# Performance work log

Measured on AMD Instinct MI355X. Metric: run time of the kernel, lower is better.

The kernel has to match this reference:

```python
import jax, jax.numpy as jnp
import numpy as np

# Model dims (match init_kwargs)
B, S, H = 1, 2048, 1024
E = 16            # n_routed_experts
I = 768           # moe_intermediate_size
TOPK = 4          # num_experts_per_tok
G = 4             # n_group
TOPK_G = 2        # topk_group
SCALE = 2.5       # routed_scaling_factor
N_SHARED = 1      # n_shared_experts


def setup_inputs() -> dict:
    key = jax.random.key(0)
    ks = jax.random.split(key, 9)
    def rn(k, shape, scale=0.02):
        return jax.random.normal(k, shape, dtype=jnp.float32) * scale
    return dict(
        hidden_states=jax.random.normal(ks[0], (B, S, H), dtype=jnp.float32),
        gate_w=rn(ks[1], (E, H)),
        gate_bias=jax.random.normal(ks[2], (E,), dtype=jnp.float32) * 0.1,
        w1=rn(ks[3], (E, I, H)),   # gate_proj weights [out,in]
        w2=rn(ks[4], (E, H, I)),   # down_proj weights
        w3=rn(ks[5], (E, I, H)),   # up_proj weights
        ws1=rn(ks[6], (I * N_SHARED, H)),
        ws2=rn(ks[7], (H, I * N_SHARED)),
        ws3=rn(ks[8], (I * N_SHARED, H)),
    )


def _route(x, gate_w, gate_bias):
    """noaux_tc routing: sigmoid scores + bias, group top-k, top_k experts."""
    n = x.shape[0]
    logits = jnp.einsum('nh,eh->ne', x.astype(jnp.float32), gate_w)  # [N,E]
    scores = jax.nn.sigmoid(logits)
    sb = scores + gate_bias                                          # biased scores
    # group score = sum of top-2 biased scores in each group
    gs = sb.reshape(n, G, E // G)
    group_scores = jnp.sum(jax.lax.top_k(gs, 2)[0], axis=-1)         # [N,G]
    _, gidx = jax.lax.top_k(group_scores, TOPK_G)                    # [N,TOPK_G]
    gmask = jnp.sum(jax.nn.one_hot(gidx, G, dtype=sb.dtype), axis=1) # [N,G]
    emask = jnp.repeat(gmask, E // G, axis=-1)                       # [N,E]
    masked = jnp.where(emask > 0, sb, -jnp.inf)
    _, tidx = jax.lax.top_k(masked, TOPK)                            # [N,TOPK]
    w = jnp.take_along_axis(scores, tidx, axis=1)                    # unbiased weights
    w = w / (jnp.sum(w, axis=-1, keepdims=True) + 1e-20)             # norm_topk_prob
    return tidx, w * SCALE


def reference(hidden_states, gate_w, gate_bias, w1, w2, w3, ws1, ws2, ws3):
    b, s, h = hidden_states.shape
    x = hidden_states.reshape(-1, h)                                 # [N,H]
    tidx, tw = _route(x, gate_w, gate_bias)
    n = x.shape[0]
    # dense combine weights [N,E] (zero for unselected experts)
    combine = jnp.zeros((n, E), x.dtype).at[jnp.arange(n)[:, None], tidx].add(tw)
    # grouped SwiGLU experts (dense-over-experts reference form)
    g = jnp.einsum('nh,eih->nei', x, w1)
    u = jnp.einsum('nh,eih->nei', x, w3)
    hact = jax.nn.silu(g) * u * combine[:, :, None]
    y = jnp.einsum('nei,ehi->nh', hact, w2)
    # shared expert SwiGLU
    shared = jnp.einsum('ni,hi->nh', jax.nn.silu(x @ ws1.T) * (x @ ws3.T), ws2)
    return (y + shared).reshape(b, s, h)
```

## Files before the change

kernel.cpp:

```cpp
#include <hip/hip_runtime.h>
#include <hip/hip_bf16.h>
#include <math.h>

#define N_TOK 2048
#define H_DIM 1024
#define N_EXP 16
#define I_DIM 768
#define TOPK 4
#define SCALE 2.5f

#define GU_SLOTS 256
#define DN_SLOTS 192
#define GU_TAB (8 * GU_SLOTS)
#define DN_TAB (8 * DN_SLOTS)
#define GU_NY (I_DIM / 64)
#define DN_NY (H_DIM / 128)
#define MAX_GRP 832

typedef __attribute__((ext_vector_type(8))) short bf16x8;
typedef __attribute__((ext_vector_type(4))) float f32x4;

#define OFF_COUNTS   0
#define OFF_OFFSETS  128
#define OFF_WGU      256
#define OFF_WDN      (OFF_WGU + GU_TAB*4)
#define OFF_TOKIDS   (OFF_WDN + DN_TAB*4)
#define OFF_TOKW     (OFF_TOKIDS + N_EXP*N_TOK*4)
#define OFF_INV      (OFF_TOKW + N_EXP*N_TOK*4)
#define OFF_XB       (OFF_INV + N_TOK*TOPK*4)
#define OFF_HACT     (OFF_XB + (size_t)N_TOK*H_DIM*2)
#define OFF_GWT      (OFF_HACT + (size_t)N_TOK*(TOPK+1)*I_DIM*2)
#define OFF_YTMP     (OFF_GWT + N_EXP*H_DIM*4)

__device__ __forceinline__ ushort f2bf(float f) {
    union { __hip_bfloat16 h; ushort u; } cv;
    cv.h = __float2bfloat16(f);
    return cv.u;
}
__device__ __forceinline__ unsigned pack2(float lo, float hi) {
    return (unsigned)f2bf(lo) | ((unsigned)f2bf(hi) << 16);
}
__device__ __forceinline__ void async_copy16(const void* g, void* l) {
    __builtin_amdgcn_global_load_lds(
        (const __attribute__((address_space(1))) unsigned int*)g,
        (__attribute__((address_space(3))) unsigned int*)l, 16, 0, 0);
}

__global__ void k_gwt(const float* __restrict__ gw, float* __restrict__ gwT) {
    int i = blockIdx.x * 256 + threadIdx.x;
    int k = i >> 4, e = i & 15;
    gwT[i] = gw[e * H_DIM + k];
}

__launch_bounds__(256)
__global__ void k_route(const float* __restrict__ x, const float* __restrict__ gwT,
                        const float* __restrict__ gb,
                        int* __restrict__ counts, int* __restrict__ tok_ids,
                        float* __restrict__ tok_w, ushort* __restrict__ xb,
                        int* __restrict__ inv) {
    __shared__ float lgs[4][N_EXP + 1];
    int tid = threadIdx.x;
    int wv = tid >> 6, lane = tid & 63;
    int e = lane & 15, ks = lane >> 4;
    int n = blockIdx.x * 4 + wv;

    const float* xr = x + (size_t)n * H_DIM + ks * 256;
    ushort* xbr = xb + (size_t)n * H_DIM + ks * 256;
    const float* wr = gwT + ks * 256 * N_EXP + e;
    float a0 = 0.f, a1 = 0.f, a2 = 0.f, a3 = 0.f;
#pragma unroll 8
    for (int k = 0; k < 256; k += 4) {
        float4 xv = *(const float4*)(xr + k);
        a0 += xv.x * wr[(k + 0) * N_EXP];
        a1 += xv.y * wr[(k + 1) * N_EXP];
        a2 += xv.z * wr[(k + 2) * N_EXP];
        a3 += xv.w * wr[(k + 3) * N_EXP];
        if (e == 0) {
            uint2 p;
            p.x = pack2(xv.x, xv.y);
            p.y = pack2(xv.z, xv.w);
            *(uint2*)(xbr + k) = p;
        }
    }
    float acc = (a0 + a1) + (a2 + a3);
    acc += __shfl_xor(acc, 16);
    acc += __shfl_xor(acc, 32);
    if (lane < 16) lgs[wv][lane] = acc;
    __syncthreads();

    if (tid < 4) {
        int n2 = blockIdx.x * 4 + tid;
        float sc[N_EXP], sb[N_EXP];
        for (int ee = 0; ee < N_EXP; ee++) {
            float l = lgs[tid][ee];
            sc[ee] = 1.f / (1.f + expf(-l));
            sb[ee] = sc[ee] + gb[ee];
        }
        float gsc[4];
        for (int g = 0; g < 4; g++) {
            float m1 = -1e30f, m2 = -1e30f;
            for (int j = 0; j < 4; j++) {
                float v = sb[4 * g + j];
                if (v > m1) { m2 = m1; m1 = v; }
                else if (v > m2) m2 = v;
            }
            gsc[g] = m1 + m2;
        }
        int g1 = 0;
        for (int g = 1; g < 4; g++) if (gsc[g] > gsc[g1]) g1 = g;
        int g2 = -1;
        for (int g = 0; g < 4; g++) {
            if (g == g1) continue;
            if (g2 < 0 || gsc[g] > gsc[g2]) g2 = g;
        }
        bool allowed[N_EXP];
        for (int ee = 0; ee < N_EXP; ee++) {
            int grp = ee >> 2;
            allowed[ee] = (grp == g1) || (grp == g2);
        }
        int chosen[TOPK];
        float wsum = 0.f;
        for (int k = 0; k < TOPK; k++) {
            int best = -1;
            for (int ee = 0; ee < N_EXP; ee++) {
                if (!allowed[ee]) continue;
                if (best < 0 || sb[ee] > sb[best]) best = ee;
            }
            chosen[k] = best;
            allowed[best] = false;
            wsum += sc[best];
        }
        float inv_w = SCALE / (wsum + 1e-20f);
        for (int k = 0; k < TOPK; k++) {
            int ee = chosen[k];
            int p = atomicAdd(&counts[ee], 1);
            tok_ids[ee * N_TOK + p] = n2;
            tok_w[ee * N_TOK + p] = sc[ee] * inv_w;
            inv[n2 * TOPK + k] = (ee << 16) | p;
        }
    }
}

__global__ void k_scan(const int* __restrict__ counts, int* __restrict__ offsets,
                       int* __restrict__ wgu, int* __restrict__ wdn) {
    __shared__ int nmt_s[20], gpe_s[20];
    __shared__ int geb[20], deb[20];
    __shared__ int gmeta[MAX_GRP];
    __shared__ int gslot[MAX_GRP];
    __shared__ int ngu_s, ntot_s;
    int tid = threadIdx.x;
    for (int i = tid; i < GU_TAB; i += 256) wgu[i] = -1;
    for (int i = tid; i < DN_TAB; i += 256) wdn[i] = -1;
    if (tid < 17) {
        int c = (tid == 16) ? N_TOK : counts[tid];
        int nm = (c + 127) >> 7;
        nmt_s[tid] = nm;
        gpe_s[tid] = (nm + 3) >> 2;
    }
    __syncthreads();
    if (tid == 0) {
        int off = 0;
        for (int e = 0; e < N_EXP; e++) { offsets[e] = off; off += counts[e]; }
        offsets[N_EXP] = off;
        int g = 0, d = 0;
        for (int e = 0; e <= N_EXP; e++) {
            geb[e] = g; g += GU_NY * gpe_s[e];
            deb[e] = d; d += DN_NY * gpe_s[e];
        }
        geb[N_EXP + 1] = g; deb[N_EXP + 1] = d;
        ngu_s = g; ntot_s = g + d;
    }
    __syncthreads();
    int ngu = ngu_s, ntot = ntot_s;
    for (int g = tid; g < ntot; g += 256) {
        bool gu = g < ngu;
        int r = gu ? g : g - ngu;
        const int* eb = gu ? geb : deb;
        int e = 0;
        while (eb[e + 1] <= r) e++;
        int rem = r - eb[e];
        int gp = gpe_s[e];
        int y = rem / gp, mc = rem - y * gp;
        int m0t = mc * 4;
        int size = nmt_s[e] - m0t; if (size > 4) size = 4;
        gmeta[g] = e | (m0t << 5) | (y << 9) | (size << 24);
    }
    __syncthreads();
    if (tid < 8) {
        int s = 0;
        for (int g = tid; g < ngu; g += 8) { gslot[g] = s; s += (gmeta[g] >> 24); }
    } else if (tid < 16) {
        int c = tid - 8, s = 0;
        for (int g = ngu + c; g < ntot; g += 8) { gslot[g] = s; s += (gmeta[g] >> 24); }
    }
    __syncthreads();
    int k = tid & 3;
    for (int g = tid >> 2; g < ntot; g += 64) {
        int p = gmeta[g];
        int size = (p >> 24);
        if (k >= size) continue;
        int desc = (p & 0x1FFF) + (k << 5);
        bool gu = g < ngu;
        int r = gu ? g : g - ngu;
        int idx = (r & 7) + 8 * (gslot[g] + k);
        if (gu) wgu[idx] = desc; else wdn[idx] = desc;
    }
}

__launch_bounds__(256, 3)
__global__ void k_gateup(const ushort* __restrict__ xb, const float* __restrict__ w1,
                         const float* __restrict__ w3, const float* __restrict__ ws1,
                         const float* __restrict__ ws3, const int* __restrict__ counts,
                         const int* __restrict__ offsets, const int* __restrict__ wgu,
                         const int* __restrict__ tok_ids, const float* __restrict__ tok_w,
                         ushort* __restrict__ hact) {
    int desc = wgu[blockIdx.x];
    if (desc < 0) return;
    int e = desc & 31;
    int m0 = ((desc >> 5) & 15) * 128;
    int i0 = ((desc >> 9) & 15) * 64;
    int Me = (e == N_EXP) ? N_TOK : counts[e];
    const float* W1 = (e == N_EXP) ? ws1 : w1 + (size_t)e * I_DIM * H_DIM;
    const float* W3 = (e == N_EXP) ? ws3 : w3 + (size_t)e * I_DIM * H_DIM;
    int base = offsets[e];

    __shared__ ushort As[128][64];
    __shared__ ushort Bs[128][64];
    __shared__ float tws[128];

    int tid = threadIdx.x;
    int wv = tid >> 6, lane = tid & 63;
    int seg = lane & 7, rsub = lane >> 3;
    int gch = (seg ^ rsub) * 8;

    if (tid < 128) {
        int r = m0 + tid;
        tws[tid] = (e == N_EXP) ? 1.f : ((r < Me) ? tok_w[e * N_TOK + r] : 0.f);
    }

    const ushort* aptr[4];
#pragma unroll
    for (int j = 0; j < 4; j++) {
        int gr = m0 + wv * 32 + j * 8 + rsub;
        int tok = (e == N_EXP) ? gr : ((gr < Me) ? tok_ids[e * N_TOK + gr] : 0);
        aptr[j] = xb + (size_t)tok * H_DIM + gch;
    }
    const float* bptrf[4];
#pragma unroll
    for (int j = 0; j < 4; j++) {
        int r = wv * 32 + j * 8 + rsub;
        const float* W = (r < 64) ? (W1 + (size_t)(i0 + r) * H_DIM)
                                  : (W3 + (size_t)(i0 + r - 64) * H_DIM);
        bptrf[j] = W + gch;
    }

    int quad = lane >> 4, lr = lane & 15, rx = lr & 7;
    f32x4 acc[2][8] = {};

    const int NK = H_DIM / 64;
    float4 bv0[4], bv1[4];
#pragma unroll
    for (int j = 0; j < 4; j++) {
        bv0[j] = *(const float4*)(bptrf[j]);
        bv1[j] = *(const float4*)(bptrf[j] + 4);
    }
    for (int k = 0; k < NK; k++) {
        int off = k * 64;
#pragma unroll
        for (int j = 0; j < 4; j++) async_copy16(aptr[j] + off, &As[wv * 32 + j * 8][0]);
#pragma unroll
        for (int j = 0; j < 4; j++) {
            uint4 p;
            p.x = pack2(bv0[j].x, bv0[j].y);
            p.y = pack2(bv0[j].z, bv0[j].w);
            p.z = pack2(bv1[j].x, bv1[j].y);
            p.w = pack2(bv1[j].z, bv1[j].w);
            *(uint4*)&Bs[wv * 32 + j * 8 + rsub][seg * 8] = p;
        }
        if (k + 1 < NK) {
#pragma unroll
            for (int j = 0; j < 4; j++) {
                bv0[j] = *(const float4*)(bptrf[j] + off + 64);
                bv1[j] = *(const float4*)(bptrf[j] + off + 68);
            }
        }
        __syncthreads();
#pragma unroll
        for (int ks = 0; ks < 2; ks++) {
            int co = ((ks * 4 + quad) ^ rx) * 8;
            bf16x8 a0 = *(const bf16x8*)&As[wv * 32 + lr][co];
            bf16x8 a1 = *(const bf16x8*)&As[wv * 32 + 16 + lr][co];
#pragma unroll
            for (int ni = 0; ni < 8; ni++) {
                bf16x8 bf = *(const bf16x8*)&Bs[ni * 16 + lr][co];
                acc[0][ni] = __builtin_amdgcn_mfma_f32_16x16x32_bf16(a0, bf, acc[0][ni], 0, 0, 0);
                acc[1][ni] = __builtin_amdgcn_mfma_f32_16x16x32_bf16(a1, bf, acc[1][ni], 0, 0, 0);
            }
        }
        __syncthreads();
    }

#pragma unroll
    for (int mi = 0; mi < 2; mi++) {
#pragma unroll
        for (int ni = 0; ni < 4; ni++) {
            f32x4 g = acc[mi][ni];
            f32x4 u = acc[mi][ni + 4];
#pragma unroll
            for (int rg = 0; rg < 4; rg++) {
                int ml = wv * 32 + mi * 16 + quad * 4 + rg;
                int row = m0 + ml;
                if (row < Me) {
                    float gg = g[rg], uu = u[rg];
                    float act = (gg / (1.f + expf(-gg))) * uu * tws[ml];
                    hact[(size_t)(base + row) * I_DIM + i0 + ni * 16 + lr] = f2bf(act);
                }
            }
        }
    }
}

__launch_bounds__(256, 3)
__global__ void k_down(const ushort* __restrict__ hact, const float* __restrict__ w2,
                       const float* __restrict__ ws2, const int* __restrict__ counts,
                       const int* __restrict__ offsets, const int* __restrict__ wdn,
                       float* __restrict__ ytmp) {
    int desc = wdn[blockIdx.x];
    if (desc < 0) return;
    int e = desc & 31;
    int m0 = ((desc >> 5) & 15) * 128;
    int h0 = ((desc >> 9) & 15) * 128;
    int Me = (e == N_EXP) ? N_TOK : counts[e];
    const float* W2 = (e == N_EXP) ? ws2 : w2 + (size_t)e * H_DIM * I_DIM;
    int base = offsets[e];

    __shared__ ushort As[128][64];
    __shared__ ushort Bs[128][64];

    int tid = threadIdx.x;
    int wv = tid >> 6, lane = tid & 63;
    int seg = lane & 7, rsub = lane >> 3;
    int gch = (seg ^ rsub) * 8;

    const ushort* aptr[4];
#pragma unroll
    for (int j = 0; j < 4; j++) {
        int row = wv * 32 + j * 8 + rsub;
        aptr[j] = hact + (size_t)(base + m0 + row) * I_DIM + gch;
    }
    const float* bptrf[4];
#pragma unroll
    for (int j = 0; j < 4; j++) {
        int r = wv * 32 + j * 8 + rsub;
        bptrf[j] = W2 + (size_t)(h0 + r) * I_DIM + gch;
    }

    int quad = lane >> 4, lr = lane & 15, rx = lr & 7;
    f32x4 acc[2][8] = {};

    const int NK = I_DIM / 64;
    float4 bv0[4], bv1[4];
#pragma unroll
    for (int j = 0; j < 4; j++) {
        bv0[j] = *(const float4*)(bptrf[j]);
        bv1[j] = *(const float4*)(bptrf[j] + 4);
    }
    for (int k = 0; k < NK; k++) {
        int off = k * 64;
#pragma unroll
        for (int j = 0; j < 4; j++) async_copy16(aptr[j] + off, &As[wv * 32 + j * 8][0]);
#pragma unroll
        for (int j = 0; j < 4; j++) {
            uint4 p;
            p.x = pack2(bv0[j].x, bv0[j].y);
            p.y = pack2(bv0[j].z, bv0[j].w);
            p.z = pack2(bv1[j].x, bv1[j].y);
            p.w = pack2(bv1[j].z, bv1[j].w);
            *(uint4*)&Bs[wv * 32 + j * 8 + rsub][seg * 8] = p;
        }
        if (k + 1 < NK) {
#pragma unroll
            for (int j = 0; j < 4; j++) {
                bv0[j] = *(const float4*)(bptrf[j] + off + 64);
                bv1[j] = *(const float4*)(bptrf[j] + off + 68);
            }
        }
        __syncthreads();
#pragma unroll
        for (int ks = 0; ks < 2; ks++) {
            int co = ((ks * 4 + quad) ^ rx) * 8;
            bf16x8 a0 = *(const bf16x8*)&As[wv * 32 + lr][co];
            bf16x8 a1 = *(const bf16x8*)&As[wv * 32 + 16 + lr][co];
#pragma unroll
            for (int ni = 0; ni < 8; ni++) {
                bf16x8 bf = *(const bf16x8*)&Bs[ni * 16 + lr][co];
                acc[0][ni] = __builtin_amdgcn_mfma_f32_16x16x32_bf16(a0, bf, acc[0][ni], 0, 0, 0);
                acc[1][ni] = __builtin_amdgcn_mfma_f32_16x16x32_bf16(a1, bf, acc[1][ni], 0, 0, 0);
            }
        }
        __syncthreads();
    }

#pragma unroll
    for (int mi = 0; mi < 2; mi++) {
#pragma unroll
        for (int ni = 0; ni < 8; ni++) {
#pragma unroll
            for (int rg = 0; rg < 4; rg++) {
                int ml = wv * 32 + mi * 16 + quad * 4 + rg;
                int row = m0 + ml;
                if (row < Me) {
                    ytmp[(size_t)(base + row) * H_DIM + h0 + ni * 16 + lr] =
                        acc[mi][ni][rg];
                }
            }
        }
    }
}

__launch_bounds__(256)
__global__ void k_reduce(const float* __restrict__ ytmp, const int* __restrict__ inv,
                         const int* __restrict__ offsets, float* __restrict__ out) {
    int t = blockIdx.x, tid = threadIdx.x;
    const float4* yt = (const float4*)ytmp;
    float4 s = yt[(size_t)(offsets[N_EXP] + t) * (H_DIM / 4) + tid];
#pragma unroll
    for (int k = 0; k < TOPK; k++) {
        int v = inv[t * TOPK + k];
        int slot = offsets[v >> 16] + (v & 0xFFFF);
        float4 a = yt[(size_t)slot * (H_DIM / 4) + tid];
        s.x += a.x; s.y += a.y; s.z += a.z; s.w += a.w;
    }
    ((float4*)out)[(size_t)t * (H_DIM / 4) + tid] = s;
}

extern "C" void kernel_launch(void* const* d_in, const int* in_sizes, int n_in,
                              void* d_out, int out_size, void* d_ws, size_t ws_size,
                              hipStream_t stream) {
    const float* x   = (const float*)d_in[0];
    const float* gw  = (const float*)d_in[1];
    const float* gb  = (const float*)d_in[2];
    const float* w1  = (const float*)d_in[3];
    const float* w2  = (const float*)d_in[4];
    const float* w3  = (const float*)d_in[5];
    const float* ws1 = (const float*)d_in[6];
    const float* ws2 = (const float*)d_in[7];
    const float* ws3 = (const float*)d_in[8];
    float* out = (float*)d_out;

    char* wsb = (char*)d_ws;
    int* counts   = (int*)(wsb + OFF_COUNTS);
    int* offsets  = (int*)(wsb + OFF_OFFSETS);
    int* wgu      = (int*)(wsb + OFF_WGU);
    int* wdn      = (int*)(wsb + OFF_WDN);
    int* tok_ids  = (int*)(wsb + OFF_TOKIDS);
    float* tok_w  = (float*)(wsb + OFF_TOKW);
    int* inv      = (int*)(wsb + OFF_INV);
    ushort* xb    = (ushort*)(wsb + OFF_XB);
    ushort* hact  = (ushort*)(wsb + OFF_HACT);
    float* gwT    = (float*)(wsb + OFF_GWT);
    float* ytmp   = (float*)(wsb + OFF_YTMP);

    hipMemsetAsync(wsb, 0, 128, stream);

    k_gwt<<<N_EXP * H_DIM / 256, 256, 0, stream>>>(gw, gwT);
    k_route<<<N_TOK / 4, 256, 0, stream>>>(x, gwT, gb, counts, tok_ids, tok_w, xb, inv);
    k_scan<<<1, 256, 0, stream>>>(counts, offsets, wgu, wdn);
    k_gateup<<<GU_TAB, 256, 0, stream>>>(xb, w1, w3, ws1, ws3, counts, offsets,
                                         wgu, tok_ids, tok_w, hact);
    k_down<<<DN_TAB, 256, 0, stream>>>(hact, w2, ws2, counts, offsets, wdn, ytmp);
    k_reduce<<<N_TOK, 256, 0, stream>>>(ytmp, inv, offsets, out);
}
```

Measured before the change: 351.4 us.

## Double-buffer A tiles in expert GEMMs and drop gate weight transpose kernel

The gate-up and down GEMM kernels now keep two A-tile buffers in shared memory. The async copy of the next A tile is issued before the MFMA work on the current tile, and the B-tile convert-and-store is moved after compute so global loads overlap the matrix math. Separately, the routing kernel reads gate weights directly with float4 loads in their original layout, which removes the k_gwt transpose launch and its workspace buffer. The cost is extra LDS per block, which may reduce occupancy under the 3-blocks-per-CU launch bound.

```diff
diff --git a/kernel.cpp b/kernel.cpp
--- a/kernel.cpp
+++ b/kernel.cpp
@@ -29,8 +29,7 @@
 #define OFF_INV      (OFF_TOKW + N_EXP*N_TOK*4)
 #define OFF_XB       (OFF_INV + N_TOK*TOPK*4)
 #define OFF_HACT     (OFF_XB + (size_t)N_TOK*H_DIM*2)
-#define OFF_GWT      (OFF_HACT + (size_t)N_TOK*(TOPK+1)*I_DIM*2)
-#define OFF_YTMP     (OFF_GWT + N_EXP*H_DIM*4)
+#define OFF_YTMP     (OFF_HACT + (size_t)N_TOK*(TOPK+1)*I_DIM*2)
 
 __device__ __forceinline__ ushort f2bf(float f) {
     union { __hip_bfloat16 h; ushort u; } cv;
@@ -46,14 +45,8 @@
         (__attribute__((address_space(3))) unsigned int*)l, 16, 0, 0);
 }
 
-__global__ void k_gwt(const float* __restrict__ gw, float* __restrict__ gwT) {
-    int i = blockIdx.x * 256 + threadIdx.x;
-    int k = i >> 4, e = i & 15;
-    gwT[i] = gw[e * H_DIM + k];
-}
-
 __launch_bounds__(256)
-__global__ void k_route(const float* __restrict__ x, const float* __restrict__ gwT,
+__global__ void k_route(const float* __restrict__ x, const float* __restrict__ gw,
                         const float* __restrict__ gb,
                         int* __restrict__ counts, int* __restrict__ tok_ids,
                         float* __restrict__ tok_w, ushort* __restrict__ xb,
@@ -66,15 +59,16 @@
 
     const float* xr = x + (size_t)n * H_DIM + ks * 256;
     ushort* xbr = xb + (size_t)n * H_DIM + ks * 256;
-    const float* wr = gwT + ks * 256 * N_EXP + e;
+    const float* wr = gw + (size_t)e * H_DIM + ks * 256;
     float a0 = 0.f, a1 = 0.f, a2 = 0.f, a3 = 0.f;
 #pragma unroll 8
     for (int k = 0; k < 256; k += 4) {
         float4 xv = *(const float4*)(xr + k);
-        a0 += xv.x * wr[(k + 0) * N_EXP];
-        a1 += xv.y * wr[(k + 1) * N_EXP];
-        a2 += xv.z * wr[(k + 2) * N_EXP];
-        a3 += xv.w * wr[(k + 3) * N_EXP];
+        float4 wvv = *(const float4*)(wr + k);
+        a0 += xv.x * wvv.x;
+        a1 += xv.y * wvv.y;
+        a2 += xv.z * wvv.z;
+        a3 += xv.w * wvv.w;
         if (e == 0) {
             uint2 p;
             p.x = pack2(xv.x, xv.y);
@@ -224,7 +218,7 @@
     const float* W3 = (e == N_EXP) ? ws3 : w3 + (size_t)e * I_DIM * H_DIM;
     int base = offsets[e];
 
-    __shared__ ushort As[128][64];
+    __shared__ ushort As[2][128][64];
     __shared__ ushort Bs[128][64];
     __shared__ float tws[128];
 
@@ -260,36 +254,40 @@
     const int NK = H_DIM / 64;
     float4 bv0[4], bv1[4];
 #pragma unroll
+    for (int j = 0; j < 4; j++) async_copy16(aptr[j], &As[0][wv * 32 + j * 8][0]);
+#pragma unroll
     for (int j = 0; j < 4; j++) {
         bv0[j] = *(const float4*)(bptrf[j]);
         bv1[j] = *(const float4*)(bptrf[j] + 4);
     }
+#pragma unroll
+    for (int j = 0; j < 4; j++) {
+        uint4 p;
+        p.x = pack2(bv0[j].x, bv0[j].y);
+        p.y = pack2(bv0[j].z, bv0[j].w);
+        p.z = pack2(bv1[j].x, bv1[j].y);
+        p.w = pack2(bv1[j].z, bv1[j].w);
+        *(uint4*)&Bs[wv * 32 + j * 8 + rsub][seg * 8] = p;
+    }
+#pragma unroll
+    for (int j = 0; j < 4; j++) {
+        bv0[j] = *(const float4*)(bptrf[j] + 64);
+        bv1[j] = *(const float4*)(bptrf[j] + 68);
+    }
+
+    int c = 0;
     for (int k = 0; k < NK; k++) {
-        int off = k * 64;
-#pragma unroll
-        for (int j = 0; j < 4; j++) async_copy16(aptr[j] + off, &As[wv * 32 + j * 8][0]);
-#pragma unroll
-        for (int j = 0; j < 4; j++) {
-            uint4 p;
-            p.x = pack2(bv0[j].x, bv0[j].y);
-            p.y = pack2(bv0[j].z, bv0[j].w);
-            p.z = pack2(bv1[j].x, bv1[j].y);
-            p.w = pack2(bv1[j].z, bv1[j].w);
-            *(uint4*)&Bs[wv * 32 + j * 8 + rsub][seg * 8] = p;
-        }
+        __syncthreads();
         if (k + 1 < NK) {
 #pragma unroll
-            for (int j = 0; j < 4; j++) {
-                bv0[j] = *(const float4*)(bptrf[j] + off + 64);
-                bv1[j] = *(const float4*)(bptrf[j] + off + 68);
-            }
-        }
-        __syncthreads();
+            for (int j = 0; j < 4; j++)
+                async_copy16(aptr[j] + (k + 1) * 64, &As[c ^ 1][wv * 32 + j * 8][0]);
+        }
 #pragma unroll
         for (int ks = 0; ks < 2; ks++) {
             int co = ((ks * 4 + quad) ^ rx) * 8;
-            bf16x8 a0 = *(const bf16x8*)&As[wv * 32 + lr][co];
-            bf16x8 a1 = *(const bf16x8*)&As[wv * 32 + 16 + lr][co];
+            bf16x8 a0 = *(const bf16x8*)&As[c][wv * 32 + lr][co];
+            bf16x8 a1 = *(const bf16x8*)&As[c][wv * 32 + 16 + lr][co];
 #pragma unroll
             for (int ni = 0; ni < 8; ni++) {
                 bf16x8 bf = *(const bf16x8*)&Bs[ni * 16 + lr][co];
@@ -298,6 +296,25 @@
             }
         }
         __syncthreads();
+        if (k + 1 < NK) {
+#pragma unroll
+            for (int j = 0; j < 4; j++) {
+                uint4 p;
+                p.x = pack2(bv0[j].x, bv0[j].y);
+                p.y = pack2(bv0[j].z, bv0[j].w);
+                p.z = pack2(bv1[j].x, bv1[j].y);
+                p.w = pack2(bv1[j].z, bv1[j].w);
+                *(uint4*)&Bs[wv * 32 + j * 8 + rsub][seg * 8] = p;
+            }
+            if (k + 2 < NK) {
+#pragma unroll
+                for (int j = 0; j < 4; j++) {
+                    bv0[j] = *(const float4*)(bptrf[j] + (k + 2) * 64);
+                    bv1[j] = *(const float4*)(bptrf[j] + (k + 2) * 64 + 4);
+                }
+            }
+        }
+        c ^= 1;
     }
 
 #pragma unroll
@@ -334,7 +351,7 @@
     const float* W2 = (e == N_EXP) ? ws2 : w2 + (size_t)e * H_DIM * I_DIM;
     int base = offsets[e];
 
-    __shared__ ushort As[128][64];
+    __shared__ ushort As[2][128][64];
     __shared__ ushort Bs[128][64];
 
     int tid = threadIdx.x;
@@ -361,36 +378,40 @@
     const int NK = I_DIM / 64;
     float4 bv0[4], bv1[4];
 #pragma unroll
+    for (int j = 0; j < 4; j++) async_copy16(aptr[j], &As[0][wv * 32 + j * 8][0]);
+#pragma unroll
     for (int j = 0; j < 4; j++) {
         bv0[j] = *(const float4*)(bptrf[j]);
         bv1[j] = *(const float4*)(bptrf[j] + 4);
     }
+#pragma unroll
+    for (int j = 0; j < 4; j++) {
+        uint4 p;
+        p.x = pack2(bv0[j].x, bv0[j].y);
+        p.y = pack2(bv0[j].z, bv0[j].w);
+        p.z = pack2(bv1[j].x, bv1[j].y);
+        p.w = pack2(bv1[j].z, bv1[j].w);
+        *(uint4*)&Bs[wv * 32 + j * 8 + rsub][seg * 8] = p;
+    }
+#pragma unroll
+    for (int j = 0; j < 4; j++) {
+        bv0[j] = *(const float4*)(bptrf[j] + 64);
+        bv1[j] = *(const float4*)(bptrf[j] + 68);
+    }
+
+    int c = 0;
     for (int k = 0; k < NK; k++) {
-        int off = k * 64;
-#pragma unroll
-        for (int j = 0; j < 4; j++) async_copy16(aptr[j] + off, &As[wv * 32 + j * 8][0]);
-#pragma unroll
-        for (int j = 0; j < 4; j++) {
-            uint4 p;
-            p.x = pack2(bv0[j].x, bv0[j].y);
-            p.y = pack2(bv0[j].z, bv0[j].w);
-            p.z = pack2(bv1[j].x, bv1[j].y);
-            p.w = pack2(bv1[j].z, bv1[j].w);
-            *(uint4*)&Bs[wv * 32 + j * 8 + rsub][seg * 8] = p;
-        }
+        __syncthreads();
         if (k + 1 < NK) {
 #pragma unroll
-            for (int j = 0; j < 4; j++) {
-                bv0[j] = *(const float4*)(bptrf[j] + off + 64);
-                bv1[j] = *(const float4*)(bptrf[j] + off + 68);
-            }
-        }
-        __syncthreads();
+            for (int j = 0; j < 4; j++)
+                async_copy16(aptr[j] + (k + 1) * 64, &As[c ^ 1][wv * 32 + j * 8][0]);
+        }
 #pragma unroll
         for (int ks = 0; ks < 2; ks++) {
             int co = ((ks * 4 + quad) ^ rx) * 8;
-            bf16x8 a0 = *(const bf16x8*)&As[wv * 32 + lr][co];
-            bf16x8 a1 = *(const bf16x8*)&As[wv * 32 + 16 + lr][co];
+            bf16x8 a0 = *(const bf16x8*)&As[c][wv * 32 + lr][co];
+            bf16x8 a1 = *(const bf16x8*)&As[c][wv * 32 + 16 + lr][co];
 #pragma unroll
             for (int ni = 0; ni < 8; ni++) {
                 bf16x8 bf = *(const bf16x8*)&Bs[ni * 16 + lr][co];
@@ -399,6 +420,25 @@
             }
         }
         __syncthreads();
+        if (k + 1 < NK) {
+#pragma unroll
+            for (int j = 0; j < 4; j++) {
+                uint4 p;
+                p.x = pack2(bv0[j].x, bv0[j].y);
+                p.y = pack2(bv0[j].z, bv0[j].w);
+                p.z = pack2(bv1[j].x, bv1[j].y);
+                p.w = pack2(bv1[j].z, bv1[j].w);
+                *(uint4*)&Bs[wv * 32 + j * 8 + rsub][seg * 8] = p;
+            }
+            if (k + 2 < NK) {
+#pragma unroll
+                for (int j = 0; j < 4; j++) {
+                    bv0[j] = *(const float4*)(bptrf[j] + (k + 2) * 64);
+                    bv1[j] = *(const float4*)(bptrf[j] + (k + 2) * 64 + 4);
+                }
+            }
+        }
+        c ^= 1;
     }
 
 #pragma unroll
@@ -458,13 +498,11 @@
     int* inv      = (int*)(wsb + OFF_INV);
     ushort* xb    = (ushort*)(wsb + OFF_XB);
     ushort* hact  = (ushort*)(wsb + OFF_HACT);
-    float* gwT    = (float*)(wsb + OFF_GWT);
     float* ytmp   = (float*)(wsb + OFF_YTMP);
 
     hipMemsetAsync(wsb, 0, 128, stream);
 
-    k_gwt<<<N_EXP * H_DIM / 256, 256, 0, stream>>>(gw, gwT);
-    k_route<<<N_TOK / 4, 256, 0, stream>>>(x, gwT, gb, counts, tok_ids, tok_w, xb, inv);
+    k_route<<<N_TOK / 4, 256, 0, stream>>>(x, gw, gb, counts, tok_ids, tok_w, xb, inv);
     k_scan<<<1, 256, 0, stream>>>(counts, offsets, wgu, wdn);
     k_gateup<<<GU_TAB, 256, 0, stream>>>(xb, w1, w3, ws1, ws3, counts, offsets,
                                          wgu, tok_ids, tok_w, hact);
```

New measurement: 357.6 us. Within noise of the previous version (+1.8%).
